# Kernel optimization log

Hardware: AMD Instinct MI355X
Metric: run time of the kernel (lower is better)

The kernel has to match this reference:

```python
import jax, jax.numpy as jnp
import numpy as np

EPS = 1e-5  # torch LayerNorm default

def _layernorm(x, g, b):
    mu = jnp.mean(x, axis=-1, keepdims=True)
    var = jnp.var(x, axis=-1, keepdims=True)
    return (x - mu) * jax.lax.rsqrt(var + EPS) * g + b

def _mlp(x, g, b, W1, b1, W2, b2):
    # pre-norm LayerNorm -> Linear -> SiLU -> Linear
    h = _layernorm(x, g, b)
    h = jax.nn.silu(h @ W1 + b1)
    return h @ W2 + b2

N, B, F, H = 500_000, 25_000, 128, 64

def setup_inputs() -> dict:
    key = jax.random.key(0)
    ks = jax.random.split(key, 16)
    s = 0.05
    return {
        "pos": jax.random.normal(ks[0], (N, 3), jnp.float32),
        "mass_center": jax.random.normal(ks[1], (B, 3), jnp.float32),
        "scaler": jax.random.normal(ks[2], (N, F), jnp.float32),
        "vector": jax.random.normal(ks[3], (N, 3, F), jnp.float32),
        "batch_index": jnp.sort(jax.random.randint(ks[4], (N,), 0, B)),
        # decoder_alpha params (pre-norm MLP F->H->1)
        "ln_a_g": jnp.ones((F,), jnp.float32),
        "ln_a_b": jnp.zeros((F,), jnp.float32),
        "Wa1": jax.random.normal(ks[5], (F, H), jnp.float32) * s,
        "ba1": jnp.zeros((H,), jnp.float32),
        "Wa2": jax.random.normal(ks[6], (H, 1), jnp.float32) * s,
        "ba2": jnp.zeros((1,), jnp.float32),
        # decoder_nu: gate MLP (pre-norm, F->H->1) + bias-free Linear(F,1)
        "ln_n_g": jnp.ones((F,), jnp.float32),
        "ln_n_b": jnp.zeros((F,), jnp.float32),
        "Wn1": jax.random.normal(ks[7], (F, H), jnp.float32) * s,
        "bn1": jnp.zeros((H,), jnp.float32),
        "Wn2": jax.random.normal(ks[8], (H, 1), jnp.float32) * s,
        "bn2": jnp.zeros((1,), jnp.float32),
        "Wnu": jax.random.normal(ks[9], (F, 1), jnp.float32) * s,
    }

def reference(pos, mass_center, scaler, vector, batch_index,
              ln_a_g, ln_a_b, Wa1, ba1, Wa2, ba2,
              ln_n_g, ln_n_b, Wn1, bn1, Wn2, bn2, Wnu):
    # gather per-node mass center and center positions: [N,3]
    mcv = pos - mass_center[batch_index]
    # Gate: mlp(scaler) [N,1] broadcast-multiplied with vector @ Wnu [N,3,1]
    s_gate = _mlp(scaler, ln_n_g, ln_n_b, Wn1, bn1, Wn2, bn2)       # [N,1]
    v_proj = jnp.einsum('ndf,fo->ndo', vector, Wnu)                  # [N,3,1]
    nu = (s_gate[:, None, :] * v_proj)[..., 0]                       # [N,3]
    # symmetric outer products: [N,3,3]
    outer = nu[:, :, None] * mcv[:, None, :] + mcv[:, :, None] * nu[:, None, :]
    alpha_s = _mlp(scaler, ln_a_g, ln_a_b, Wa1, ba1, Wa2, ba2)       # [N,1]
    alpha = alpha_s[:, :, None] * jnp.eye(3, dtype=alpha_s.dtype) + outer  # [N,3,3]
    # scatter-sum to molecule level, then trace/3
    mol = jax.ops.segment_sum(alpha, batch_index, num_segments=B)    # [B,3,3]
    out = jnp.einsum('bii->b', mol) / 3.0
    return out[:, None]                                              # [B,1]
```

## Files before the change

kernel.cpp:

```cpp
#include <hip/hip_runtime.h>

#define FD 128
#define HD 64
#define NC 128
#define RPB 64

typedef __attribute__((ext_vector_type(8))) short bf16x8;
typedef __attribute__((ext_vector_type(4))) float f32x4;

__device__ __forceinline__ unsigned bfr(float x) {
    unsigned u = __float_as_uint(x);
    return (u + 0x7fffu + ((u >> 16) & 1u)) >> 16;
}

__device__ __forceinline__ f32x4 ntload4(const float* p) {
    return __builtin_nontemporal_load(reinterpret_cast<const f32x4*>(p));
}

__global__ void prep_kernel(
    const float* __restrict__ lnag, const float* __restrict__ lnab,
    const float* __restrict__ Wa1, const float* __restrict__ ba1, const float* __restrict__ Wa2,
    const float* __restrict__ lnng, const float* __restrict__ lnnb,
    const float* __restrict__ Wn1, const float* __restrict__ bn1, const float* __restrict__ Wn2,
    unsigned short* __restrict__ wq, float* __restrict__ c, float* __restrict__ w2)
{
    int n = threadIdx.x;
    const float* W  = (n < HD) ? Wa1 : Wn1;
    const float* g  = (n < HD) ? lnag : lnng;
    const float* bb = (n < HD) ? lnab : lnnb;
    const float* b1 = (n < HD) ? ba1 : bn1;
    const float* W2 = (n < HD) ? Wa2 : Wn2;
    int h = n & (HD - 1);
    float accb = b1[h];
    for (int f = 0; f < FD; ++f) {
        float w = W[f * HD + h];
        wq[n * FD + f] = (unsigned short)bfr(g[f] * w);
        accb += bb[f] * w;
    }
    c[n] = accb;
    w2[n] = W2[h];
}

__global__ __launch_bounds__(256, 4) void fused_kernel(
    const float* __restrict__ scaler, const float* __restrict__ vec,
    const float* __restrict__ wnu, const float* __restrict__ pos,
    const float* __restrict__ mc, const int* __restrict__ bidx,
    const unsigned short* __restrict__ wq, const float* __restrict__ c,
    const float* __restrict__ w2, const float* __restrict__ ba2,
    const float* __restrict__ bn2, float* __restrict__ val, int n_nodes)
{
    __shared__ float tl[4][16];

    int tid = threadIdx.x;
    int lane = tid & 63, w = tid >> 6;
    int rowbase = blockIdx.x * RPB + w * 16;
    int lrow = lane & 15, lgrp = lane >> 4;

    int xnode = rowbase + lrow;
    int gx = xnode < n_nodes ? xnode : (n_nodes - 1);
    const float* xp = scaler + (size_t)gx * FD;
    f32x4 xv[8];
#pragma unroll
    for (int ks = 0; ks < 4; ++ks) {
        xv[2 * ks]     = ntload4(xp + (ks * 8 + lgrp * 2) * 4);
        xv[2 * ks + 1] = ntload4(xp + (ks * 8 + lgrp * 2 + 1) * 4);
    }

    {
        int o = lane >> 3, cc = lane & 7;
        f32x4 wn4[4];
#pragma unroll
        for (int m = 0; m < 4; ++m)
            wn4[m] = *reinterpret_cast<const f32x4*>(wnu + (m * 8 + cc) * 4);
#pragma unroll
        for (int g = 0; g < 2; ++g) {
            int row = g * 8 + o;
            int node = rowbase + row;
            int n = node < n_nodes ? node : (n_nodes - 1);
            int b = bidx[n];
            float m0 = pos[n * 3 + 0] - mc[b * 3 + 0];
            float m1 = pos[n * 3 + 1] - mc[b * 3 + 1];
            float m2 = pos[n * 3 + 2] - mc[b * 3 + 2];
            const float* vr = vec + (size_t)n * 3 * FD;
            float acc = 0.f;
#pragma unroll
            for (int k = 0; k < 12; ++k) {
                f32x4 v = ntload4(vr + (cc + k * 8) * 4);
                f32x4 wnv = wn4[k & 3];
                float d4 = v.x * wnv.x + v.y * wnv.y + v.z * wnv.z + v.w * wnv.w;
                float mm = (k < 4) ? m0 : (k < 8 ? m1 : m2);
                acc = fmaf(d4, mm, acc);
            }
            acc += __shfl_xor(acc, 1);
            acc += __shfl_xor(acc, 2);
            acc += __shfl_xor(acc, 4);
            if (cc == 0) tl[w][row] = acc;
        }
    }

    float s = 0.f, s2 = 0.f;
#pragma unroll
    for (int i = 0; i < 8; ++i) {
        f32x4 v = xv[i];
        s  += v.x + v.y + v.z + v.w;
        s2 += v.x * v.x + v.y * v.y + v.z * v.z + v.w * v.w;
    }
    s  += __shfl_xor(s, 16);  s  += __shfl_xor(s, 32);
    s2 += __shfl_xor(s2, 16); s2 += __shfl_xor(s2, 32);
    float mu = s * (1.f / FD);
    float var = s2 * (1.f / FD) - mu * mu;
    float rstd = rsqrtf(var + 1e-5f);

    bf16x8 af[4];
#pragma unroll
    for (int ks = 0; ks < 4; ++ks) {
        f32x4 a = xv[2 * ks], b = xv[2 * ks + 1];
        union { unsigned u[4]; bf16x8 v; } pk;
        pk.u[0] = bfr((a.x - mu) * rstd) | (bfr((a.y - mu) * rstd) << 16);
        pk.u[1] = bfr((a.z - mu) * rstd) | (bfr((a.w - mu) * rstd) << 16);
        pk.u[2] = bfr((b.x - mu) * rstd) | (bfr((b.y - mu) * rstd) << 16);
        pk.u[3] = bfr((b.z - mu) * rstd) | (bfr((b.w - mu) * rstd) << 16);
        af[ks] = pk.v;
    }

    float pa[4] = {0.f, 0.f, 0.f, 0.f}, pn[4] = {0.f, 0.f, 0.f, 0.f};
#pragma unroll
    for (int tp = 0; tp < 4; ++tp) {
        f32x4 a0 = {0.f, 0.f, 0.f, 0.f}, a1 = {0.f, 0.f, 0.f, 0.f};
        int n0 = (2 * tp) * 16 + lrow, n1 = (2 * tp + 1) * 16 + lrow;
        const bf16x8* brow0 = reinterpret_cast<const bf16x8*>(wq + n0 * FD);
        const bf16x8* brow1 = reinterpret_cast<const bf16x8*>(wq + n1 * FD);
#pragma unroll
        for (int ks = 0; ks < 4; ++ks) {
            bf16x8 bf0 = brow0[ks * 4 + lgrp];
            bf16x8 bf1 = brow1[ks * 4 + lgrp];
            a0 = __builtin_amdgcn_mfma_f32_16x16x32_bf16(af[ks], bf0, a0, 0, 0, 0);
            a1 = __builtin_amdgcn_mfma_f32_16x16x32_bf16(af[ks], bf1, a1, 0, 0, 0);
        }
#pragma unroll
        for (int half = 0; half < 2; ++half) {
            f32x4 acc = half ? a1 : a0;
            int tc = 2 * tp + half;
            int col = tc * 16 + lrow;
            float bias = c[col], w2v = w2[col];
#pragma unroll
            for (int r = 0; r < 4; ++r) {
                float h1 = acc[r] + bias;
                float y = h1 / (1.f + __expf(-h1));
                float cb = y * w2v;
                if (tc < 4) pa[r] += cb; else pn[r] += cb;
            }
        }
    }
#pragma unroll
    for (int off = 1; off < 16; off <<= 1) {
#pragma unroll
        for (int r = 0; r < 4; ++r) {
            pa[r] += __shfl_xor(pa[r], off);
            pn[r] += __shfl_xor(pn[r], off);
        }
    }
    if (lrow == 0) {
        float b2a = ba2[0], b2n = bn2[0];
        float tmp[4];
#pragma unroll
        for (int r = 0; r < 4; ++r) {
            int nl = lgrp * 4 + r;
            tmp[r] = (pa[r] + b2a) + (2.f / 3.f) * (pn[r] + b2n) * tl[w][nl];
        }
        int node0 = rowbase + lgrp * 4;
        if (node0 + 3 < n_nodes) {
            f32x4 o4 = {tmp[0], tmp[1], tmp[2], tmp[3]};
            *reinterpret_cast<f32x4*>(val + node0) = o4;
        } else {
#pragma unroll
            for (int r = 0; r < 4; ++r)
                if (node0 + r < n_nodes) val[node0 + r] = tmp[r];
        }
    }
}

__global__ __launch_bounds__(256) void reduce_kernel(
    const float* __restrict__ val, const int* __restrict__ bidx,
    float* __restrict__ out, int n_nodes, int n_batch)
{
    int b = (int)(blockIdx.x * blockDim.x + threadIdx.x);
    if (b >= n_batch) return;
    int lo = 0, hi = n_nodes;
    while (lo < hi) { int mid = (lo + hi) >> 1; if (bidx[mid] < b) lo = mid + 1; else hi = mid; }
    int s0 = lo;
    hi = n_nodes;
    while (lo < hi) { int mid = (lo + hi) >> 1; if (bidx[mid] <= b) lo = mid + 1; else hi = mid; }
    float acc = 0.f;
    for (int i = s0; i < lo; ++i) acc += val[i];
    out[b] = acc;
}

extern "C" void kernel_launch(void* const* d_in, const int* in_sizes, int n_in,
                              void* d_out, int out_size, void* d_ws, size_t ws_size,
                              hipStream_t stream) {
    const float* pos    = (const float*)d_in[0];
    const float* mc     = (const float*)d_in[1];
    const float* scaler = (const float*)d_in[2];
    const float* vec    = (const float*)d_in[3];
    const int*   bidx   = (const int*)d_in[4];
    const float* lnag   = (const float*)d_in[5];
    const float* lnab   = (const float*)d_in[6];
    const float* Wa1    = (const float*)d_in[7];
    const float* ba1    = (const float*)d_in[8];
    const float* Wa2    = (const float*)d_in[9];
    const float* ba2    = (const float*)d_in[10];
    const float* lnng   = (const float*)d_in[11];
    const float* lnnb   = (const float*)d_in[12];
    const float* Wn1    = (const float*)d_in[13];
    const float* bn1    = (const float*)d_in[14];
    const float* Wn2    = (const float*)d_in[15];
    const float* bn2    = (const float*)d_in[16];
    const float* Wnu    = (const float*)d_in[17];

    int N = in_sizes[0] / 3;
    int B = in_sizes[1] / 3;

    unsigned short* wq = (unsigned short*)d_ws;
    float* c  = (float*)((char*)d_ws + NC * FD * 2);
    float* w2 = c + NC;
    float* val = w2 + NC;

    hipLaunchKernelGGL(prep_kernel, dim3(1), dim3(NC), 0, stream,
                       lnag, lnab, Wa1, ba1, Wa2, lnng, lnnb, Wn1, bn1, Wn2, wq, c, w2);

    int blocks = (N + RPB - 1) / RPB;
    hipLaunchKernelGGL(fused_kernel, dim3(blocks), dim3(256), 0, stream,
                       scaler, vec, Wnu, pos, mc, bidx, wq, c, w2, ba2, bn2,
                       val, N);

    int rblocks = (B + 255) / 256;
    hipLaunchKernelGGL(reduce_kernel, dim3(rblocks), dim3(256), 0, stream,
                       val, bidx, (float*)d_out, N, B);
}
```

Measured before the change: 233.3 us.

## Parallelize weight prep and replace per-segment binary search with boundary kernel

The single-block weight-prep kernel becomes one block per hidden unit with a shuffle reduction, so the serial 128-iteration loop is spread across threads. A new kernel builds segment start offsets from the sorted batch index in one pass. The reduce kernel then reads these offsets instead of running two binary searches per molecule, and sums with four-way unrolled accumulators. This adds one launch and an extra pass over the batch index in exchange for shorter serial prep and cheaper segment lookup.

```diff
diff --git a/kernel.cpp b/kernel.cpp
--- a/kernel.cpp
+++ b/kernel.cpp
@@ -17,28 +17,47 @@
     return __builtin_nontemporal_load(reinterpret_cast<const f32x4*>(p));
 }
 
-__global__ void prep_kernel(
+__global__ __launch_bounds__(128) void prep_kernel(
     const float* __restrict__ lnag, const float* __restrict__ lnab,
     const float* __restrict__ Wa1, const float* __restrict__ ba1, const float* __restrict__ Wa2,
     const float* __restrict__ lnng, const float* __restrict__ lnnb,
     const float* __restrict__ Wn1, const float* __restrict__ bn1, const float* __restrict__ Wn2,
     unsigned short* __restrict__ wq, float* __restrict__ c, float* __restrict__ w2)
 {
-    int n = threadIdx.x;
+    int n = blockIdx.x;
+    int f = threadIdx.x;
     const float* W  = (n < HD) ? Wa1 : Wn1;
     const float* g  = (n < HD) ? lnag : lnng;
     const float* bb = (n < HD) ? lnab : lnnb;
     const float* b1 = (n < HD) ? ba1 : bn1;
     const float* W2 = (n < HD) ? Wa2 : Wn2;
     int h = n & (HD - 1);
-    float accb = b1[h];
-    for (int f = 0; f < FD; ++f) {
-        float w = W[f * HD + h];
-        wq[n * FD + f] = (unsigned short)bfr(g[f] * w);
-        accb += bb[f] * w;
-    }
-    c[n] = accb;
-    w2[n] = W2[h];
+    float w = W[f * HD + h];
+    wq[n * FD + f] = (unsigned short)bfr(g[f] * w);
+    float partial = bb[f] * w;
+#pragma unroll
+    for (int off = 32; off; off >>= 1) partial += __shfl_xor(partial, off);
+    __shared__ float ps[2];
+    if ((f & 63) == 0) ps[f >> 6] = partial;
+    __syncthreads();
+    if (f == 0) { c[n] = ps[0] + ps[1] + b1[h]; w2[n] = W2[h]; }
+}
+
+__global__ __launch_bounds__(256) void bound_kernel(
+    const int* __restrict__ bidx, int* __restrict__ start, int n_nodes, int n_batch)
+{
+    int i = (int)(blockIdx.x * blockDim.x + threadIdx.x);
+    if (i >= n_nodes) return;
+    int b = bidx[i];
+    if (i == 0) {
+        for (int x = 0; x <= b; ++x) start[x] = 0;
+    } else {
+        int pb = bidx[i - 1];
+        for (int x = pb + 1; x <= b; ++x) start[x] = i;
+    }
+    if (i == n_nodes - 1) {
+        for (int x = b + 1; x <= n_batch; ++x) start[x] = n_nodes;
+    }
 }
 
 __global__ __launch_bounds__(256, 4) void fused_kernel(
@@ -181,19 +200,18 @@
 }
 
 __global__ __launch_bounds__(256) void reduce_kernel(
-    const float* __restrict__ val, const int* __restrict__ bidx,
-    float* __restrict__ out, int n_nodes, int n_batch)
+    const float* __restrict__ val, const int* __restrict__ start,
+    float* __restrict__ out, int n_batch)
 {
     int b = (int)(blockIdx.x * blockDim.x + threadIdx.x);
     if (b >= n_batch) return;
-    int lo = 0, hi = n_nodes;
-    while (lo < hi) { int mid = (lo + hi) >> 1; if (bidx[mid] < b) lo = mid + 1; else hi = mid; }
-    int s0 = lo;
-    hi = n_nodes;
-    while (lo < hi) { int mid = (lo + hi) >> 1; if (bidx[mid] <= b) lo = mid + 1; else hi = mid; }
-    float acc = 0.f;
-    for (int i = s0; i < lo; ++i) acc += val[i];
-    out[b] = acc;
+    int i = start[b], e = start[b + 1];
+    float a0 = 0.f, a1 = 0.f, a2 = 0.f, a3 = 0.f;
+    for (; i + 4 <= e; i += 4) {
+        a0 += val[i]; a1 += val[i + 1]; a2 += val[i + 2]; a3 += val[i + 3];
+    }
+    for (; i < e; ++i) a0 += val[i];
+    out[b] = (a0 + a1) + (a2 + a3);
 }
 
 extern "C" void kernel_launch(void* const* d_in, const int* in_sizes, int n_in,
@@ -225,9 +243,14 @@
     float* c  = (float*)((char*)d_ws + NC * FD * 2);
     float* w2 = c + NC;
     float* val = w2 + NC;
-
-    hipLaunchKernelGGL(prep_kernel, dim3(1), dim3(NC), 0, stream,
+    int* start = (int*)(val + N);
+
+    hipLaunchKernelGGL(prep_kernel, dim3(NC), dim3(FD), 0, stream,
                        lnag, lnab, Wa1, ba1, Wa2, lnng, lnnb, Wn1, bn1, Wn2, wq, c, w2);
+
+    int bblocks = (N + 255) / 256;
+    hipLaunchKernelGGL(bound_kernel, dim3(bblocks), dim3(256), 0, stream,
+                       bidx, start, N, B);
 
     int blocks = (N + RPB - 1) / RPB;
     hipLaunchKernelGGL(fused_kernel, dim3(blocks), dim3(256), 0, stream,
@@ -236,5 +259,5 @@
 
     int rblocks = (B + 255) / 256;
     hipLaunchKernelGGL(reduce_kernel, dim3(rblocks), dim3(256), 0, stream,
-                       val, bidx, (float*)d_out, N, B);
-}
+                       val, start, (float*)d_out, B);
+}
```

Measured after the change: 222.2 us, median of 2. 1.05x faster.
